# Kernel tuning notes

Hardware: AMD Instinct MI355X
Metric: run time of the kernel (lower is better)

The kernel has to match this reference:

```python
import jax, jax.numpy as jnp
import numpy as np

# decoded layout constants
NN, NO, SD = 16, 8, 4          # num_neighbors, num_obstacles, state_dim_per_agent
B = 131072                      # batch rows
H1, E, HP, AD = 64, 16, 64, 2   # phi hidden, embed, psi hidden, action dim
D_ROBOT, D_OBST = 0.3, 0.3
B_GAMMA, B_EXPH = 0.05, 1.0
PHI_MIN, PHI_MAX = -2.0, 2.0
A_MAX = 2.0


def setup_inputs() -> dict:
    key = jax.random.key(0)
    kx, kw = jax.random.split(key)
    # x: [count | goal(SD) | NN neighbor rel-states (SD each) | NO obstacle rel-pos (2 each)]
    x = jax.random.normal(kx, (B, 1 + SD + SD * NN + 2 * NO), dtype=jnp.float32) * 2.0
    x = x.at[:, 0].set(float(NN))
    names = [("Wp1n", (SD, H1)), ("bp1n", (H1,)), ("Wp2n", (H1, E)), ("bp2n", (E,)),
             ("Wr1n", (E, H1)), ("br1n", (H1,)), ("Wr2n", (H1, E)), ("br2n", (E,)),
             ("Wp1o", (2, H1)), ("bp1o", (H1,)), ("Wp2o", (H1, E)), ("bp2o", (E,)),
             ("Wr1o", (E, H1)), ("br1o", (H1,)), ("Wr2o", (H1, E)), ("br2o", (E,)),
             ("Wpsi1", (2 * E + SD, HP)), ("bpsi1", (HP,)), ("Wpsi2", (HP, AD)), ("bpsi2", (AD,))]
    ks = jax.random.split(kw, len(names))
    inp = {"x": x}
    for (n, sh), k in zip(names, ks):
        s = 1.0 / np.sqrt(sh[0])  # torch Linear default init scale
        inp[n] = jax.random.uniform(k, sh, jnp.float32, -s, s)
    return inp


def _mlp2(h, W1, b1, W2, b2):
    # Feedforward: activation between layers, linear output
    return jax.nn.relu(h @ W1 + b1) @ W2 + b2


def _deepset(el, Wp1, bp1, Wp2, bp2, Wr1, br1, Wr2, br2):
    # el: [B, n, d] -> phi each element, sum over set, rho
    phi = _mlp2(el, Wp1, bp1, Wp2, bp2)          # [B, n, E]
    return _mlp2(phi.sum(axis=1), Wr1, br1, Wr2, br2)  # [B, E]


def _barrier_sum(P, D):
    # P: [B, n, 2]; APF barrier gamma * P / (|P| * (|P|-D)^exph), summed over n
    nrm = jnp.linalg.norm(P, axis=-1, keepdims=True)   # [B, n, 1]
    H = nrm - D
    return (B_GAMMA * P / (nrm * H ** B_EXPH)).sum(axis=1)  # [B, 2]


def reference(x, Wp1n, bp1n, Wp2n, bp2n, Wr1n, br1n, Wr2n, br2n,
              Wp1o, bp1o, Wp2o, bp2o, Wr1o, br1o, Wr2o, br2o,
              Wpsi1, bpsi1, Wpsi2, bpsi2):
    nb = x.shape[0]
    g = x[:, 1:1 + SD]                                        # goal
    nbr = x[:, 1 + SD:1 + SD + SD * NN].reshape(nb, NN, SD)   # neighbor rel-states
    obs = x[:, 1 + SD + SD * NN:].reshape(nb, NO, 2)          # obstacle rel-pos

    rho_n = _deepset(nbr, Wp1n, bp1n, Wp2n, bp2n, Wr1n, br1n, Wr2n, br2n)
    rho_o = _deepset(obs, Wp1o, bp1o, Wp2o, bp2o, Wr1o, br1o, Wr2o, br2o)

    h = jnp.concatenate([rho_n, rho_o, g], axis=1)            # [B, 2E+SD]
    emp = _mlp2(h, Wpsi1, bpsi1, Wpsi2, bpsi2)                # psi network
    emp = (jnp.tanh(emp) + 1.0) / 2.0 * (PHI_MAX - PHI_MIN) + PHI_MIN  # scale_empty

    bar = _barrier_sum(-nbr[:, :, :2], D_ROBOT) + _barrier_sum(-obs, D_OBST)

    action = emp + bar
    # scale(): divide rows whose inf-norm exceeds a_max
    inv_alpha = jnp.maximum(jnp.max(jnp.abs(action), axis=1, keepdims=True) / A_MAX, 1.0)
    return action / inv_alpha
```

## Files before the change

kernel.cpp:

```cpp
#include <hip/hip_runtime.h>
#include <math.h>


typedef __attribute__((ext_vector_type(8))) _Float16 f16x8;
typedef __attribute__((ext_vector_type(2))) __fp16 fp16x2;
typedef __attribute__((ext_vector_type(4))) float f32x4;

#define XW 85

#define FR_S1N  0
#define FR_S1O  4
#define FR_FN   8
#define FR_FO   16
#define FR_ZN   24
#define FR_ZO   32
#define FR_WG   40
#define FR_PSI2 44
#define N_FRAGS 46

#define BIG_STR 144
#define L_BIG  0
#define L_BIG2 2304
#define L_OUT  4608
#define L_BAR  4736
#define L_OBA  4864
#define GRP_LDS 5440
#define NBA_STR 136
#define OBA_STR 68

#define H16_ONE 0x00003C00u

__device__ __forceinline__ float fast_rcp(float x)  { return __builtin_amdgcn_rcpf(x); }
__device__ __forceinline__ float fast_sqrt(float x) { return __builtin_amdgcn_sqrtf(x); }

__device__ __forceinline__ float two_tanh(float a) {
    float ax = fabsf(a);
    float e = __expf(2.0f * ax);
    float t = 1.0f - 2.0f * fast_rcp(e + 1.0f);
    return copysignf(2.0f * t, a);
}

__device__ __forceinline__ void lds_order() {
    __asm__ __volatile__("" ::: "memory");
}

__device__ __forceinline__ unsigned pk2(float a, float b) {
    union { fp16x2 h; unsigned u; } t;
    t.h = __builtin_amdgcn_cvt_pkrtz(a, b);
    return t.u;
}
__device__ __forceinline__ f16x8 lds_af(const char* area, int stride, int off, int lane) {
    int mm = lane & 15, qq = lane >> 4;
    return *(const f16x8*)(area + mm * stride + off + qq * 16);
}
__device__ __forceinline__ f16x8 load_bh(const _Float16* wsf, int frag, int lane) {
    return ((const f16x8*)(wsf + (size_t)frag * 512))[lane];
}
__device__ __forceinline__ f32x4 cinit(float b) {
    f32x4 c; c[0] = b; c[1] = b; c[2] = b; c[3] = b; return c;
}
__device__ __forceinline__ f32x4 mfma1(f16x8 a, f16x8 b, f32x4 c) {
    return __builtin_amdgcn_mfma_f32_16x16x32_f16(a, b, c, 0, 0, 0);
}

__global__ void bn_prep(const float* __restrict__ Wp1n, const float* __restrict__ Wp2n,
                        const float* __restrict__ Wr1n, const float* __restrict__ Wr2n,
                        const float* __restrict__ Wp1o, const float* __restrict__ Wp2o,
                        const float* __restrict__ Wr1o, const float* __restrict__ Wr2o,
                        const float* __restrict__ Wpsi1, const float* __restrict__ Wpsi2,
                        const float* __restrict__ bp1n, const float* __restrict__ bp1o,
                        const float* __restrict__ bp2n, const float* __restrict__ bp2o,
                        const float* __restrict__ br1n, const float* __restrict__ br1o,
                        const float* __restrict__ br2n, const float* __restrict__ br2o,
                        const float* __restrict__ bpsi1,
                        _Float16* __restrict__ wsf)
{
    int f = blockIdx.x;
    int lane = threadIdx.x;
    int q = lane >> 4, c = lane & 15;

    if (f >= N_FRAGS) {
        float* dst = (float*)(wsf + (size_t)N_FRAGS * 512) + (f - N_FRAGS) * 64;
        if (lane < 64) {
            float s = 0.f;
            if (f == N_FRAGS) {
                for (int e = 0; e < 16; ++e) s = fmaf(bp2n[e], Wr1n[e * 64 + lane], s);
                dst[lane] = 16.f * s + br1n[lane];
            } else {
                for (int e = 0; e < 16; ++e) s = fmaf(bp2o[e], Wr1o[e * 64 + lane], s);
                dst[lane] = 8.f * s + br1o[lane];
            }
        }
        return;
    }

    _Float16* dstf = wsf + (size_t)f * 512 + lane * 8;

    if (f < 8) {
        const float* W   = (f < 4) ? Wp1n : Wp1o;
        const float* bia = (f < 4) ? bp1n : bp1o;
        int K  = (f < 4) ? 4 : 2;
        int nt = f & 3;
        for (int j = 0; j < 8; ++j) {
            int k = q * 8 + j;
            int n = nt * 16 + c;
            float v = 0.f;
            if (k < K) v = W[k * 64 + n];
            else if (k == K) v = bia[n];
            dstf[j] = (_Float16)v;
        }
    } else if (f < 24) {
        int rel = (f - 8) & 7;
        bool isN = f < 16;
        const float* Wa = isN ? Wp2n : Wp2o;
        const float* Wb = isN ? Wr1n : Wr1o;
        int kk = rel >> 2, nt = rel & 3;
        for (int j = 0; j < 8; ++j) {
            int k = kk * 32 + q * 8 + j;
            int n = nt * 16 + c;
            float s = 0.f;
            for (int e = 0; e < 16; ++e) s = fmaf(Wa[k * 16 + e], Wb[e * 64 + n], s);
            dstf[j] = (_Float16)(0.5f * s);
        }
    } else if (f < 40) {
        int rel = (f - 24) & 7;
        bool isN = f < 32;
        const float* Wa = isN ? Wr2n : Wr2o;
        int roff = isN ? 0 : 16;
        int kk = rel >> 2, nt = rel & 3;
        for (int j = 0; j < 8; ++j) {
            int k = kk * 32 + q * 8 + j;
            int n = nt * 16 + c;
            float s = 0.f;
            for (int e = 0; e < 16; ++e) s = fmaf(Wa[k * 16 + e], Wpsi1[(roff + e) * 64 + n], s);
            dstf[j] = (_Float16)s;
        }
    } else if (f < 44) {
        int nt = f - 40;
        for (int j = 0; j < 8; ++j) {
            int k = q * 8 + j;
            int n = nt * 16 + c;
            float v = 0.f;
            if (k < 4) v = Wpsi1[(32 + k) * 64 + n];
            else if (k == 4) {
                float s = bpsi1[n];
                for (int e = 0; e < 16; ++e) {
                    s = fmaf(br2n[e], Wpsi1[e * 64 + n], s);
                    s = fmaf(br2o[e], Wpsi1[(16 + e) * 64 + n], s);
                }
                v = s;
            }
            dstf[j] = (_Float16)v;
        }
    } else {
        int kk = f - 44;
        for (int j = 0; j < 8; ++j) {
            int k = kk * 32 + q * 8 + j;
            float v = (c < 2) ? Wpsi2[k * 2 + c] : 0.f;
            dstf[j] = (_Float16)v;
        }
    }
}

__global__ __launch_bounds__(256, 5) void bn_main(
    const float* __restrict__ x, const _Float16* __restrict__ wsf,
    const float* __restrict__ bpsi2,
    float* __restrict__ out, int nb)
{
    __shared__ char smem[4 * GRP_LDS];
    const int lane = threadIdx.x & 63;
    const int wid  = threadIdx.x >> 6;
    const int group = blockIdx.x * 4 + wid;
    const int row0 = group * 16;

    char* Gl   = smem + wid * GRP_LDS;
    char* BIG  = Gl + L_BIG;
    char* BIG2 = Gl + L_BIG2;
    char* OUTA = Gl + L_OUT;
    char* BAR  = Gl + L_BAR;
    char* OBA  = Gl + L_OBA;
    char* NBA  = BIG;

    const int m = lane & 15, q = lane >> 4, c = m;
    const float* xg   = x + (size_t)row0 * XW;
    const float* xrow = xg + (size_t)m * XW;

    const float* BFN = (const float*)(wsf + (size_t)N_FRAGS * 512);
    const float* BFO = BFN + 64;

    const f32x4 ZC = cinit(0.f);

    {
        int ln5 = lane >> 5;
        int pr  = lane & 31;
        int mm0 = pr >> 1, fp = pr & 1;
        char* db = NBA + mm0 * NBA_STR + fp * 4;
        const float* s0 = xg + (size_t)ln5 * XW + 5 + pr * 2;
        #pragma unroll
        for (int t = 0; t < 8; ++t) {
            const float* s = s0 + (size_t)(2 * t) * XW;
            *(unsigned*)(db + (2 * t + ln5) * 8) = pk2(s[0], s[1]);
        }
    }
    {
        int r8 = lane >> 3;
        int oo = lane & 7;
        char* db = OBA + oo * OBA_STR;
        const float* s0 = xg + (size_t)r8 * XW + 69 + oo * 2;
        #pragma unroll
        for (int t = 0; t < 2; ++t) {
            const float* s = s0 + (size_t)(8 * t) * XW;
            *(unsigned*)(db + (8 * t + r8) * 4) = pk2(s[0], s[1]);
        }
    }

    {
        float bx = 0.f, by = 0.f;
        #pragma unroll
        for (int i = 0; i < 4; ++i) {
            int n = 4 * q + i;
            float px = -xrow[5 + 4 * n], py = -xrow[6 + 4 * n];
            float nrm = fast_sqrt(px * px + py * py);
            float coef = 0.05f * fast_rcp(nrm * (nrm - 0.3f));
            bx = fmaf(coef, px, bx);
            by = fmaf(coef, py, by);
        }
        #pragma unroll
        for (int i = 0; i < 2; ++i) {
            int o = 2 * q + i;
            float px = -xrow[69 + 2 * o], py = -xrow[70 + 2 * o];
            float nrm = fast_sqrt(px * px + py * py);
            float coef = 0.05f * fast_rcp(nrm * (nrm - 0.3f));
            bx = fmaf(coef, px, bx);
            by = fmaf(coef, py, by);
        }
        bx += __shfl_xor(bx, 16); by += __shfl_xor(by, 16);
        bx += __shfl_xor(bx, 32); by += __shfl_xor(by, 32);
        if (q == 0) { float2 bb; bb.x = bx; bb.y = by; *(float2*)(BAR + m * 8) = bb; }
    }
    lds_order();

    {
        f16x8 Bs1n[4];
        #pragma unroll
        for (int nt = 0; nt < 4; ++nt) Bs1n[nt] = load_bh(wsf, FR_S1N + nt, lane);

        const int m8 = m * 8;
        f32x4 accS[4], accA[4];
        #pragma unroll
        for (int nt = 0; nt < 4; ++nt) { accS[nt] = cinit(0.f); accA[nt] = cinit(0.f); }
        union { f16x8 v; unsigned u[4]; uint2 h[2]; } A;
        A.u[2] = H16_ONE; A.u[3] = 0;
        #pragma unroll
        for (int mm = 0; mm < 16; ++mm) {
            A.h[0] = *(const uint2*)(NBA + mm * NBA_STR + m8);
            #pragma unroll
            for (int nt = 0; nt < 4; ++nt) {
                accS[nt] = mfma1(A.v, Bs1n[nt], accS[nt]);
                f32x4 cc = mfma1(A.v, Bs1n[nt], ZC);
                #pragma unroll
                for (int reg = 0; reg < 4; ++reg)
                    accA[nt][reg] += fabsf(cc[reg]);
            }
        }
        lds_order();
        #pragma unroll
        for (int nt = 0; nt < 4; ++nt)
            #pragma unroll
            for (int reg = 0; reg < 4; ++reg)
                *(_Float16*)(BIG + (q * 4 + reg) * BIG_STR + (nt * 16 + c) * 2)
                    = (_Float16)(accS[nt][reg] + accA[nt][reg]);
    }
    lds_order();

    {
        f16x8 Bs1o[4];
        #pragma unroll
        for (int nt = 0; nt < 4; ++nt) Bs1o[nt] = load_bh(wsf, FR_S1O + nt, lane);

        const int m4 = m * 4;
        f32x4 accS[4], accA[4];
        #pragma unroll
        for (int nt = 0; nt < 4; ++nt) { accS[nt] = cinit(0.f); accA[nt] = cinit(0.f); }
        union { f16x8 v; unsigned u[4]; } A;
        A.u[1] = H16_ONE; A.u[2] = 0; A.u[3] = 0;
        #pragma unroll
        for (int oo = 0; oo < 8; ++oo) {
            A.u[0] = *(const unsigned*)(OBA + oo * OBA_STR + m4);
            #pragma unroll
            for (int nt = 0; nt < 4; ++nt) {
                accS[nt] = mfma1(A.v, Bs1o[nt], accS[nt]);
                f32x4 cc = mfma1(A.v, Bs1o[nt], ZC);
                #pragma unroll
                for (int reg = 0; reg < 4; ++reg)
                    accA[nt][reg] += fabsf(cc[reg]);
            }
        }
        #pragma unroll
        for (int nt = 0; nt < 4; ++nt)
            #pragma unroll
            for (int reg = 0; reg < 4; ++reg)
                *(_Float16*)(BIG2 + (q * 4 + reg) * BIG_STR + (nt * 16 + c) * 2)
                    = (_Float16)(accS[nt][reg] + accA[nt][reg]);
    }
    lds_order();

    {
        f16x8 A0 = lds_af(BIG, BIG_STR, 0, lane);
        f16x8 A1 = lds_af(BIG, BIG_STR, 64, lane);
        lds_order();
        #pragma unroll
        for (int nt = 0; nt < 4; ++nt) {
            f16x8 B0 = load_bh(wsf, FR_FN + nt, lane);
            f16x8 B1 = load_bh(wsf, FR_FN + 4 + nt, lane);
            f32x4 cc = mfma1(A0, B0, cinit(BFN[nt * 16 + c]));
            cc = mfma1(A1, B1, cc);
            #pragma unroll
            for (int reg = 0; reg < 4; ++reg)
                *(_Float16*)(BIG + (q * 4 + reg) * BIG_STR + (nt * 16 + c) * 2)
                    = (_Float16)fmaxf(cc[reg], 0.f);
        }
    }
    lds_order();

    {
        f16x8 A0 = lds_af(BIG2, BIG_STR, 0, lane);
        f16x8 A1 = lds_af(BIG2, BIG_STR, 64, lane);
        lds_order();
        #pragma unroll
        for (int nt = 0; nt < 4; ++nt) {
            f16x8 B0 = load_bh(wsf, FR_FO + nt, lane);
            f16x8 B1 = load_bh(wsf, FR_FO + 4 + nt, lane);
            f32x4 cc = mfma1(A0, B0, cinit(BFO[nt * 16 + c]));
            cc = mfma1(A1, B1, cc);
            #pragma unroll
            for (int reg = 0; reg < 4; ++reg)
                *(_Float16*)(BIG2 + (q * 4 + reg) * BIG_STR + (nt * 16 + c) * 2)
                    = (_Float16)fmaxf(cc[reg], 0.f);
        }
    }
    lds_order();

    {
        union { f16x8 v; unsigned u[4]; } gA;
        gA.u[0] = pk2(xrow[1], xrow[2]);
        gA.u[1] = pk2(xrow[3], xrow[4]);
        gA.u[2] = H16_ONE;
        gA.u[3] = 0;

        f16x8 An0 = lds_af(BIG,  BIG_STR, 0, lane);
        f16x8 An1 = lds_af(BIG,  BIG_STR, 64, lane);
        f16x8 Ao0 = lds_af(BIG2, BIG_STR, 0, lane);
        f16x8 Ao1 = lds_af(BIG2, BIG_STR, 64, lane);
        lds_order();
        #pragma unroll
        for (int nt = 0; nt < 4; ++nt) {
            f16x8 Bg  = load_bh(wsf, FR_WG + nt, lane);
            f16x8 Bn0 = load_bh(wsf, FR_ZN + nt, lane);
            f16x8 Bn1 = load_bh(wsf, FR_ZN + 4 + nt, lane);
            f16x8 Bo0 = load_bh(wsf, FR_ZO + nt, lane);
            f16x8 Bo1 = load_bh(wsf, FR_ZO + 4 + nt, lane);
            f32x4 cc = mfma1(gA.v, Bg, ZC);
            cc = mfma1(An0, Bn0, cc);
            cc = mfma1(An1, Bn1, cc);
            cc = mfma1(Ao0, Bo0, cc);
            cc = mfma1(Ao1, Bo1, cc);
            #pragma unroll
            for (int reg = 0; reg < 4; ++reg)
                *(_Float16*)(BIG + (q * 4 + reg) * BIG_STR + (nt * 16 + c) * 2)
                    = (_Float16)fmaxf(cc[reg], 0.f);
        }
    }
    lds_order();

    {
        float b_p2 = (c < 2) ? bpsi2[c] : 0.f;
        f16x8 Bp20 = load_bh(wsf, FR_PSI2 + 0, lane);
        f16x8 Bp21 = load_bh(wsf, FR_PSI2 + 1, lane);
        f16x8 A0 = lds_af(BIG, BIG_STR, 0, lane);
        f16x8 A1 = lds_af(BIG, BIG_STR, 64, lane);
        f32x4 ca = mfma1(A0, Bp20, cinit(b_p2));
        f32x4 cb = mfma1(A1, Bp21, ZC);
        if (c < 2) {
            #pragma unroll
            for (int reg = 0; reg < 4; ++reg)
                *(float*)(OUTA + (q * 4 + reg) * 8 + c * 4) = ca[reg] + cb[reg];
        }
    }
    lds_order();

    if (lane < 16) {
        float2 a  = *(const float2*)(OUTA + lane * 8);
        float2 bb = *(const float2*)(BAR + lane * 8);
        float a0 = two_tanh(a.x) + bb.x;
        float a1 = two_tanh(a.y) + bb.y;
        float amax = fmaxf(fabsf(a0), fabsf(a1));
        float inv_alpha = fmaxf(amax * 0.5f, 1.0f);
        float rr = fast_rcp(inv_alpha);
        float2 o; o.x = a0 * rr; o.y = a1 * rr;
        *(float2*)(out + (size_t)(row0 + lane) * 2) = o;
    }
}

extern "C" void kernel_launch(void* const* d_in, const int* in_sizes, int n_in,
                              void* d_out, int out_size, void* d_ws, size_t ws_size,
                              hipStream_t stream) {
    const float* x     = (const float*)d_in[0];
    const float* Wp1n  = (const float*)d_in[1];
    const float* bp1n  = (const float*)d_in[2];
    const float* Wp2n  = (const float*)d_in[3];
    const float* bp2n  = (const float*)d_in[4];
    const float* Wr1n  = (const float*)d_in[5];
    const float* br1n  = (const float*)d_in[6];
    const float* Wr2n  = (const float*)d_in[7];
    const float* br2n  = (const float*)d_in[8];
    const float* Wp1o  = (const float*)d_in[9];
    const float* bp1o  = (const float*)d_in[10];
    const float* Wp2o  = (const float*)d_in[11];
    const float* bp2o  = (const float*)d_in[12];
    const float* Wr1o  = (const float*)d_in[13];
    const float* br1o  = (const float*)d_in[14];
    const float* Wr2o  = (const float*)d_in[15];
    const float* br2o  = (const float*)d_in[16];
    const float* Wpsi1 = (const float*)d_in[17];
    const float* bpsi1 = (const float*)d_in[18];
    const float* Wpsi2 = (const float*)d_in[19];
    const float* bpsi2 = (const float*)d_in[20];
    float* out = (float*)d_out;

    int nb = in_sizes[0] / XW;
    _Float16* wsf = (_Float16*)d_ws;

    bn_prep<<<N_FRAGS + 2, 64, 0, stream>>>(Wp1n, Wp2n, Wr1n, Wr2n,
                                            Wp1o, Wp2o, Wr1o, Wr2o,
                                            Wpsi1, Wpsi2,
                                            bp1n, bp1o, bp2n, bp2o,
                                            br1n, br1o, br2n, br2o,
                                            bpsi1, wsf);

    int groups = (nb + 15) / 16;
    int blocks = (groups + 3) / 4;
    bn_main<<<blocks, 256, 0, stream>>>(x, wsf, bpsi2, out, nb);
}
```

Measured before the change: 140.3 us.

## Sum pre-activation set elements via one wide-K MFMA and fuse rho layers

The phi first-layer relu is split as (v+|v|)/2. The signed sum over set elements is now computed with a single K-stacked MFMA using new replicated weight fragments and a pre-scaled bias, instead of accumulating one MFMA per element. Obstacle inputs are kept in registers rather than staged through LDS, which shrinks per-group LDS. The neighbor and obstacle rho first layers are merged into one stage, removing a barrier round. This cuts MFMA count and LDS traffic at the cost of extra prep fragments and higher register pressure.

After: 138.1 us. About the same (-1.6%).

```diff
diff --git a/kernel.cpp b/kernel.cpp
--- a/kernel.cpp
+++ b/kernel.cpp
@@ -16,17 +16,17 @@
 #define FR_ZO   32
 #define FR_WG   40
 #define FR_PSI2 44
-#define N_FRAGS 46
+#define FR_SPN  46
+#define FR_SPO  50
+#define N_FRAGS 54
 
 #define BIG_STR 144
 #define L_BIG  0
 #define L_BIG2 2304
 #define L_OUT  4608
 #define L_BAR  4736
-#define L_OBA  4864
-#define GRP_LDS 5440
+#define GRP_LDS 4864
 #define NBA_STR 136
-#define OBA_STR 68
 
 #define H16_ONE 0x00003C00u
 
@@ -82,13 +82,18 @@
     if (f >= N_FRAGS) {
         float* dst = (float*)(wsf + (size_t)N_FRAGS * 512) + (f - N_FRAGS) * 64;
         if (lane < 64) {
-            float s = 0.f;
             if (f == N_FRAGS) {
+                float s = 0.f;
                 for (int e = 0; e < 16; ++e) s = fmaf(bp2n[e], Wr1n[e * 64 + lane], s);
                 dst[lane] = 16.f * s + br1n[lane];
-            } else {
+            } else if (f == N_FRAGS + 1) {
+                float s = 0.f;
                 for (int e = 0; e < 16; ++e) s = fmaf(bp2o[e], Wr1o[e * 64 + lane], s);
                 dst[lane] = 8.f * s + br1o[lane];
+            } else if (f == N_FRAGS + 2) {
+                dst[lane] = 16.f * bp1n[lane];
+            } else {
+                dst[lane] = 8.f * bp1o[lane];
             }
         }
         return;
@@ -152,11 +157,26 @@
             }
             dstf[j] = (_Float16)v;
         }
-    } else {
+    } else if (f < 46) {
         int kk = f - 44;
         for (int j = 0; j < 8; ++j) {
             int k = kk * 32 + q * 8 + j;
             float v = (c < 2) ? Wpsi2[k * 2 + c] : 0.f;
+            dstf[j] = (_Float16)v;
+        }
+    } else if (f < 50) {
+        int nt = f - 46;
+        for (int j = 0; j < 8; ++j) {
+            int k = q * 8 + j;
+            int n = nt * 16 + c;
+            dstf[j] = (_Float16)Wp1n[(k & 3) * 64 + n];
+        }
+    } else {
+        int nt = f - 50;
+        for (int j = 0; j < 8; ++j) {
+            int k = q * 8 + j;
+            int n = nt * 16 + c;
+            float v = (k < 16) ? Wp1o[(k & 1) * 64 + n] : 0.f;
             dstf[j] = (_Float16)v;
         }
     }
@@ -178,7 +198,6 @@
     char* BIG2 = Gl + L_BIG2;
     char* OUTA = Gl + L_OUT;
     char* BAR  = Gl + L_BAR;
-    char* OBA  = Gl + L_OBA;
     char* NBA  = BIG;
 
     const int m = lane & 15, q = lane >> 4, c = m;
@@ -187,6 +206,8 @@
 
     const float* BFN = (const float*)(wsf + (size_t)N_FRAGS * 512);
     const float* BFO = BFN + 64;
+    const float* BSN = BFN + 128;
+    const float* BSO = BFN + 192;
 
     const f32x4 ZC = cinit(0.f);
 
@@ -202,17 +223,17 @@
             *(unsigned*)(db + (2 * t + ln5) * 8) = pk2(s[0], s[1]);
         }
     }
-    {
-        int r8 = lane >> 3;
-        int oo = lane & 7;
-        char* db = OBA + oo * OBA_STR;
-        const float* s0 = xg + (size_t)r8 * XW + 69 + oo * 2;
-        #pragma unroll
-        for (int t = 0; t < 2; ++t) {
-            const float* s = s0 + (size_t)(8 * t) * XW;
-            *(unsigned*)(db + (8 * t + r8) * 4) = pk2(s[0], s[1]);
-        }
-    }
+
+    union { f16x8 v; unsigned u[4]; } gA;
+    gA.u[0] = pk2(xrow[1], xrow[2]);
+    gA.u[1] = pk2(xrow[3], xrow[4]);
+    gA.u[2] = H16_ONE;
+    gA.u[3] = 0;
+
+    unsigned obs[8];
+    #pragma unroll
+    for (int t = 0; t < 8; ++t)
+        obs[t] = pk2(xrow[69 + 2 * t], xrow[70 + 2 * t]);
 
     {
         float bx = 0.f, by = 0.f;
@@ -238,17 +259,69 @@
         bx += __shfl_xor(bx, 32); by += __shfl_xor(by, 32);
         if (q == 0) { float2 bb; bb.x = bx; bb.y = by; *(float2*)(BAR + m * 8) = bb; }
     }
+
+    {
+        f16x8 Bspo[4], Bs1o[4];
+        #pragma unroll
+        for (int nt = 0; nt < 4; ++nt) {
+            Bspo[nt] = load_bh(wsf, FR_SPO + nt, lane);
+            Bs1o[nt] = load_bh(wsf, FR_S1O + nt, lane);
+        }
+        union { f16x8 v; unsigned u[4]; } Apo;
+        Apo.u[0] = q == 0 ? obs[0] : (q == 1 ? obs[4] : 0u);
+        Apo.u[1] = q == 0 ? obs[1] : (q == 1 ? obs[5] : 0u);
+        Apo.u[2] = q == 0 ? obs[2] : (q == 1 ? obs[6] : 0u);
+        Apo.u[3] = q == 0 ? obs[3] : (q == 1 ? obs[7] : 0u);
+
+        f32x4 accS[4], accA[4];
+        #pragma unroll
+        for (int nt = 0; nt < 4; ++nt) {
+            accS[nt] = mfma1(Apo.v, Bspo[nt], cinit(BSO[nt * 16 + c]));
+            accA[nt] = cinit(0.f);
+        }
+        union { f16x8 v; unsigned u[4]; } A;
+        A.u[1] = H16_ONE; A.u[2] = 0; A.u[3] = 0;
+        #pragma unroll
+        for (int oo = 0; oo < 8; ++oo) {
+            A.u[0] = obs[oo];
+            #pragma unroll
+            for (int nt = 0; nt < 4; ++nt) {
+                f32x4 cc = mfma1(A.v, Bs1o[nt], ZC);
+                #pragma unroll
+                for (int reg = 0; reg < 4; ++reg)
+                    accA[nt][reg] += fabsf(cc[reg]);
+            }
+        }
+        #pragma unroll
+        for (int nt = 0; nt < 4; ++nt)
+            #pragma unroll
+            for (int reg = 0; reg < 4; ++reg)
+                *(_Float16*)(BIG2 + (q * 4 + reg) * BIG_STR + (nt * 16 + c) * 2)
+                    = (_Float16)(accS[nt][reg] + accA[nt][reg]);
+    }
     lds_order();
 
     {
-        f16x8 Bs1n[4];
-        #pragma unroll
-        for (int nt = 0; nt < 4; ++nt) Bs1n[nt] = load_bh(wsf, FR_S1N + nt, lane);
-
+        f16x8 Bspn[4], Bs1n[4];
+        #pragma unroll
+        for (int nt = 0; nt < 4; ++nt) {
+            Bspn[nt] = load_bh(wsf, FR_SPN + nt, lane);
+            Bs1n[nt] = load_bh(wsf, FR_S1N + nt, lane);
+        }
         const int m8 = m * 8;
+        union { f16x8 v; uint2 h[2]; } Ap0, Ap1;
+        Ap0.h[0] = *(const uint2*)(NBA + (2 * q) * NBA_STR + m8);
+        Ap0.h[1] = *(const uint2*)(NBA + (2 * q + 1) * NBA_STR + m8);
+        Ap1.h[0] = *(const uint2*)(NBA + (2 * q + 8) * NBA_STR + m8);
+        Ap1.h[1] = *(const uint2*)(NBA + (2 * q + 9) * NBA_STR + m8);
+
         f32x4 accS[4], accA[4];
         #pragma unroll
-        for (int nt = 0; nt < 4; ++nt) { accS[nt] = cinit(0.f); accA[nt] = cinit(0.f); }
+        for (int nt = 0; nt < 4; ++nt) {
+            accS[nt] = mfma1(Ap1.v, Bspn[nt],
+                       mfma1(Ap0.v, Bspn[nt], cinit(BSN[nt * 16 + c])));
+            accA[nt] = cinit(0.f);
+        }
         union { f16x8 v; unsigned u[4]; uint2 h[2]; } A;
         A.u[2] = H16_ONE; A.u[3] = 0;
         #pragma unroll
@@ -256,7 +329,6 @@
             A.h[0] = *(const uint2*)(NBA + mm * NBA_STR + m8);
             #pragma unroll
             for (int nt = 0; nt < 4; ++nt) {
-                accS[nt] = mfma1(A.v, Bs1n[nt], accS[nt]);
                 f32x4 cc = mfma1(A.v, Bs1n[nt], ZC);
                 #pragma unroll
                 for (int reg = 0; reg < 4; ++reg)
@@ -274,85 +346,36 @@
     lds_order();
 
     {
-        f16x8 Bs1o[4];
-        #pragma unroll
-        for (int nt = 0; nt < 4; ++nt) Bs1o[nt] = load_bh(wsf, FR_S1O + nt, lane);
-
-        const int m4 = m * 4;
-        f32x4 accS[4], accA[4];
-        #pragma unroll
-        for (int nt = 0; nt < 4; ++nt) { accS[nt] = cinit(0.f); accA[nt] = cinit(0.f); }
-        union { f16x8 v; unsigned u[4]; } A;
-        A.u[1] = H16_ONE; A.u[2] = 0; A.u[3] = 0;
-        #pragma unroll
-        for (int oo = 0; oo < 8; ++oo) {
-            A.u[0] = *(const unsigned*)(OBA + oo * OBA_STR + m4);
-            #pragma unroll
-            for (int nt = 0; nt < 4; ++nt) {
-                accS[nt] = mfma1(A.v, Bs1o[nt], accS[nt]);
-                f32x4 cc = mfma1(A.v, Bs1o[nt], ZC);
-                #pragma unroll
-                for (int reg = 0; reg < 4; ++reg)
-                    accA[nt][reg] += fabsf(cc[reg]);
-            }
-        }
-        #pragma unroll
-        for (int nt = 0; nt < 4; ++nt)
-            #pragma unroll
-            for (int reg = 0; reg < 4; ++reg)
-                *(_Float16*)(BIG2 + (q * 4 + reg) * BIG_STR + (nt * 16 + c) * 2)
-                    = (_Float16)(accS[nt][reg] + accA[nt][reg]);
-    }
-    lds_order();
-
-    {
-        f16x8 A0 = lds_af(BIG, BIG_STR, 0, lane);
-        f16x8 A1 = lds_af(BIG, BIG_STR, 64, lane);
-        lds_order();
-        #pragma unroll
-        for (int nt = 0; nt < 4; ++nt) {
-            f16x8 B0 = load_bh(wsf, FR_FN + nt, lane);
-            f16x8 B1 = load_bh(wsf, FR_FN + 4 + nt, lane);
-            f32x4 cc = mfma1(A0, B0, cinit(BFN[nt * 16 + c]));
-            cc = mfma1(A1, B1, cc);
-            #pragma unroll
-            for (int reg = 0; reg < 4; ++reg)
-                *(_Float16*)(BIG + (q * 4 + reg) * BIG_STR + (nt * 16 + c) * 2)
-                    = (_Float16)fmaxf(cc[reg], 0.f);
-        }
-    }
-    lds_order();
-
-    {
-        f16x8 A0 = lds_af(BIG2, BIG_STR, 0, lane);
-        f16x8 A1 = lds_af(BIG2, BIG_STR, 64, lane);
-        lds_order();
-        #pragma unroll
-        for (int nt = 0; nt < 4; ++nt) {
-            f16x8 B0 = load_bh(wsf, FR_FO + nt, lane);
-            f16x8 B1 = load_bh(wsf, FR_FO + 4 + nt, lane);
-            f32x4 cc = mfma1(A0, B0, cinit(BFO[nt * 16 + c]));
-            cc = mfma1(A1, B1, cc);
-            #pragma unroll
-            for (int reg = 0; reg < 4; ++reg)
-                *(_Float16*)(BIG2 + (q * 4 + reg) * BIG_STR + (nt * 16 + c) * 2)
-                    = (_Float16)fmaxf(cc[reg], 0.f);
-        }
-    }
-    lds_order();
-
-    {
-        union { f16x8 v; unsigned u[4]; } gA;
-        gA.u[0] = pk2(xrow[1], xrow[2]);
-        gA.u[1] = pk2(xrow[3], xrow[4]);
-        gA.u[2] = H16_ONE;
-        gA.u[3] = 0;
-
         f16x8 An0 = lds_af(BIG,  BIG_STR, 0, lane);
         f16x8 An1 = lds_af(BIG,  BIG_STR, 64, lane);
         f16x8 Ao0 = lds_af(BIG2, BIG_STR, 0, lane);
         f16x8 Ao1 = lds_af(BIG2, BIG_STR, 64, lane);
-        lds_order();
+        #pragma unroll
+        for (int nt = 0; nt < 4; ++nt) {
+            f16x8 Bn0 = load_bh(wsf, FR_FN + nt, lane);
+            f16x8 Bn1 = load_bh(wsf, FR_FN + 4 + nt, lane);
+            f32x4 cn = mfma1(An0, Bn0, cinit(BFN[nt * 16 + c]));
+            cn = mfma1(An1, Bn1, cn);
+            f16x8 Bo0 = load_bh(wsf, FR_FO + nt, lane);
+            f16x8 Bo1 = load_bh(wsf, FR_FO + 4 + nt, lane);
+            f32x4 co = mfma1(Ao0, Bo0, cinit(BFO[nt * 16 + c]));
+            co = mfma1(Ao1, Bo1, co);
+            #pragma unroll
+            for (int reg = 0; reg < 4; ++reg) {
+                *(_Float16*)(BIG + (q * 4 + reg) * BIG_STR + (nt * 16 + c) * 2)
+                    = (_Float16)fmaxf(cn[reg], 0.f);
+                *(_Float16*)(BIG2 + (q * 4 + reg) * BIG_STR + (nt * 16 + c) * 2)
+                    = (_Float16)fmaxf(co[reg], 0.f);
+            }
+        }
+    }
+    lds_order();
+
+    {
+        f16x8 An0 = lds_af(BIG,  BIG_STR, 0, lane);
+        f16x8 An1 = lds_af(BIG,  BIG_STR, 64, lane);
+        f16x8 Ao0 = lds_af(BIG2, BIG_STR, 0, lane);
+        f16x8 Ao1 = lds_af(BIG2, BIG_STR, 64, lane);
         #pragma unroll
         for (int nt = 0; nt < 4; ++nt) {
             f16x8 Bg  = load_bh(wsf, FR_WG + nt, lane);
@@ -431,7 +454,7 @@
     int nb = in_sizes[0] / XW;
     _Float16* wsf = (_Float16*)d_ws;
 
-    bn_prep<<<N_FRAGS + 2, 64, 0, stream>>>(Wp1n, Wp2n, Wr1n, Wr2n,
+    bn_prep<<<N_FRAGS + 4, 64, 0, stream>>>(Wp1n, Wp2n, Wr1n, Wr2n,
                                             Wp1o, Wp2o, Wr1o, Wr2o,
                                             Wpsi1, Wpsi2,
                                             bp1n, bp1o, bp2n, bp2o,
```
